# Performance work log

Measured on AMD Instinct MI355X. Metric: run time of the kernel, lower is better.

The kernel has to match this reference:

```python
import jax, jax.numpy as jnp
import numpy as np
import math

B, T, M, C, H = 2, 2048, 77, 512, 8
D = C // H  # head dim = 64


def setup_inputs() -> dict:
    key = jax.random.key(0)
    ks = jax.random.split(key, 20)
    s = 0.02
    inp = {
        "x": jax.random.normal(ks[0], (B, T, C), jnp.float32),
        "c": jax.random.normal(ks[1], (B, M, C), jnp.float32),
        # causal mask for self-attention (masked_fill where == 0)
        "attn_mask": jnp.tril(jnp.ones((T, T), jnp.int32))[None, None],
        "padding_mask": jnp.ones((B, M), jnp.int32),
    }
    names = ["Wq", "Wk", "Wv", "Wkc", "Wvc", "Wg1", "Wg2", "Wp"]
    for i, n in enumerate(names):
        inp[n] = jax.random.normal(ks[2 + i], (C, C), jnp.float32) * s
        inp["b" + n[1:]] = jnp.zeros((C,), jnp.float32)
    return inp


def _heads(t):
    # [B, S, C] -> [B, S, H, D]
    return t.reshape(t.shape[0], t.shape[1], H, D)


def reference(x, c, attn_mask, padding_mask,
              Wq, bq, Wk, bk, Wv, bv, Wkc, bkc, Wvc, bvc,
              Wg1, bg1, Wg2, bg2, Wp, bp):
    scale = 1.0 / math.sqrt(D)
    q = _heads(x @ Wq + bq)      # [B,T,H,D]
    k = _heads(x @ Wk + bk)      # [B,T,H,D]
    v = _heads(x @ Wv + bv)
    k_c = _heads(c @ Wkc + bkc)  # [B,M,H,D]
    v_c = _heads(c @ Wvc + bvc)

    # self-attention branch
    att = jnp.einsum("bthd,bshd->bhts", q, k) * scale   # [B,H,T,T]
    att = jnp.where(attn_mask == 0, -jnp.inf, att)
    att = jax.nn.softmax(att, axis=-1)
    y = jnp.einsum("bhts,bshd->bthd", att, v).reshape(B, T, C)

    # cross-attention branch to condition c
    att_c = jnp.einsum("bthd,bmhd->bhtm", q, k_c) * scale  # [B,H,T,M]
    att_c = jnp.where(padding_mask[:, None, None, :] == 0, -jnp.inf, att_c)
    att_c = jax.nn.softmax(att_c, axis=-1)
    y_c = jnp.einsum("bhtm,bmhd->bthd", att_c, v_c).reshape(B, T, C)

    # sigmoid gating fusion (note: gates cross-multiply branches, per source)
    gate_self = jax.nn.sigmoid(y @ Wg1 + bg1)
    gate_c = jax.nn.sigmoid(y_c @ Wg2 + bg2)
    y = gate_self * y_c + gate_c * y
    return y @ Wp + bp
```

## Files before the change

kernel.cpp:

```cpp
#include <hip/hip_runtime.h>
#include <hip/hip_bf16.h>
#include <math.h>

#define BB 2
#define TT 2048
#define MM 77
#define CC 512
#define HH 8
#define DD 64

typedef short bf16x8 __attribute__((ext_vector_type(8)));
typedef float f32x4  __attribute__((ext_vector_type(4)));

static __device__ __forceinline__ unsigned short f2bf(float x) {
    __hip_bfloat16 h = __float2bfloat16(x);
    return *reinterpret_cast<unsigned short*>(&h);
}
static __device__ __forceinline__ float bf2f(unsigned short u) {
    unsigned int v = ((unsigned int)u) << 16;
    return *reinterpret_cast<float*>(&v);
}

__global__ __launch_bounds__(256)
void wconv8(const float* __restrict__ w0, const float* __restrict__ w1,
            const float* __restrict__ w2, const float* __restrict__ w3,
            const float* __restrict__ w4, const float* __restrict__ w5,
            const float* __restrict__ w6, const float* __restrict__ w7,
            unsigned short* __restrict__ outbase)
{
    const float* W;
    switch (blockIdx.z) {
        case 0: W = w0; break; case 1: W = w1; break;
        case 2: W = w2; break; case 3: W = w3; break;
        case 4: W = w4; break; case 5: W = w5; break;
        case 6: W = w6; break; default: W = w7; break;
    }
    unsigned short* Wp = outbase + (size_t)blockIdx.z * 512 * 512;
    const int k0 = blockIdx.x * 64;
    const int n0 = blockIdx.y * 64;
    const int tid = threadIdx.x;
    __shared__ unsigned short t[64 * 72];

    #pragma unroll
    for (int it = 0; it < 4; ++it) {
        const int e = tid + 256 * it;
        const int r  = e >> 4;
        const int c4 = (e & 15) * 4;
        const float4 v = *(const float4*)(W + (size_t)(k0 + r) * 512 + n0 + c4);
        t[(c4 + 0) * 72 + r] = f2bf(v.x);
        t[(c4 + 1) * 72 + r] = f2bf(v.y);
        t[(c4 + 2) * 72 + r] = f2bf(v.z);
        t[(c4 + 3) * 72 + r] = f2bf(v.w);
    }
    __syncthreads();
    #pragma unroll
    for (int it = 0; it < 2; ++it) {
        const int e    = tid + 256 * it;
        const int gl   = e >> 7;
        const int ktl  = (e >> 6) & 1;
        const int lane = e & 63;
        const int l15  = lane & 15;
        const int q    = lane >> 4;
        const int4 v = *(const int4*)&t[(gl * 16 + l15) * 72 + ktl * 32 + q * 8];
        const int G  = (n0 >> 4) + gl;
        const int KT = (k0 >> 5) + ktl;
        *(int4*)(Wp + ((size_t)(G * 16 + KT) * 64 + lane) * 8) = v;
    }
}

__global__ __launch_bounds__(256)
void proj_all(const float* __restrict__ x, const float* __restrict__ cin,
              const unsigned short* __restrict__ Wt8,
              const float* __restrict__ bq, const float* __restrict__ bk,
              const float* __restrict__ bv, const float* __restrict__ bkc,
              const float* __restrict__ bvc,
              unsigned short* __restrict__ qb, unsigned short* __restrict__ kcb)
{
    __shared__ unsigned short As[2 * 16 * 64 * 8];

    const int tid = threadIdx.x;
    int b = blockIdx.x;
    const float* Ap; const unsigned short* Wtp;
    const float *bb0, *bb1, *bb2;
    unsigned short* outb;
    int row0, colb, N, S, whichStride;
    float oscale;
    if (b < 768) {
        row0 = (b & 127) * 32; colb = (b >> 7) * 256;
        Ap = x; Wtp = Wt8; N = BB * TT; S = TT;
        whichStride = 2097152; oscale = 0.125f;
        outb = qb; bb0 = bq; bb1 = bk; bb2 = bv;
    } else {
        b -= 768;
        row0 = (b % 5) * 32; colb = (b / 5) * 256;
        Ap = cin; Wtp = Wt8 + 3 * 262144; N = BB * MM; S = MM;
        whichStride = 131072; oscale = 1.0f;
        outb = kcb; bb0 = bkc; bb1 = bvc; bb2 = nullptr;
    }

    {
        const int r    = tid >> 3;
        const int rg   = r >> 4;
        const int l15r = r & 15;
        const int seg  = (tid & 7) * 64;
        const int gr   = row0 + r;
        unsigned short tmp[64];
        #pragma unroll
        for (int j = 0; j < 16; ++j) {
            float4 v = (gr < N) ? *(const float4*)(Ap + (size_t)gr * 512 + seg + j * 4)
                                : make_float4(0.f, 0.f, 0.f, 0.f);
            tmp[j*4+0] = f2bf(v.x); tmp[j*4+1] = f2bf(v.y);
            tmp[j*4+2] = f2bf(v.z); tmp[j*4+3] = f2bf(v.w);
        }
        #pragma unroll
        for (int jb = 0; jb < 8; ++jb) {
            const int k  = seg + jb * 8;
            const int kt = k >> 5;
            const int q  = (k >> 3) & 3;
            *(int4*)&As[((rg * 16 + kt) * 64 + q * 16 + l15r) * 8] = *(int4*)&tmp[jb*8];
        }
    }
    __syncthreads();

    const int wv   = tid >> 6;
    const int lane = tid & 63;
    const int l15  = lane & 15;
    const int quad = lane >> 4;
    const int wc   = colb + wv * 64;
    const int wcg  = wc >> 4;

    f32x4 acc[2][4];
    #pragma unroll
    for (int mi = 0; mi < 2; ++mi)
        #pragma unroll
        for (int ni = 0; ni < 4; ++ni) acc[mi][ni] = (f32x4){0.f, 0.f, 0.f, 0.f};

    bf16x8 b0v[4], b1v[4], b2v[4];
    #pragma unroll
    for (int ni = 0; ni < 4; ++ni) {
        b0v[ni] = *(const bf16x8*)(Wtp + (((size_t)(wcg + ni) * 16 + 0) << 9) + lane * 8);
        b1v[ni] = *(const bf16x8*)(Wtp + (((size_t)(wcg + ni) * 16 + 1) << 9) + lane * 8);
    }

    for (int kt = 0; kt < 16; ++kt) {
        if (kt + 2 < 16) {
            #pragma unroll
            for (int ni = 0; ni < 4; ++ni)
                b2v[ni] = *(const bf16x8*)(Wtp + (((size_t)(wcg + ni) * 16 + kt + 2) << 9) + lane * 8);
        }
        const bf16x8 a0 = *(const bf16x8*)&As[((0 * 16 + kt) * 64 + lane) * 8];
        const bf16x8 a1 = *(const bf16x8*)&As[((1 * 16 + kt) * 64 + lane) * 8];
        #pragma unroll
        for (int ni = 0; ni < 4; ++ni) {
            acc[0][ni] = __builtin_amdgcn_mfma_f32_16x16x32_bf16(a0, b0v[ni], acc[0][ni], 0, 0, 0);
            acc[1][ni] = __builtin_amdgcn_mfma_f32_16x16x32_bf16(a1, b0v[ni], acc[1][ni], 0, 0, 0);
        }
        #pragma unroll
        for (int ni = 0; ni < 4; ++ni) { b0v[ni] = b1v[ni]; b1v[ni] = b2v[ni]; }
    }

    const int which = wc >> 9;
    const float* bsel = (which == 0) ? bb0 : ((which == 1) ? bb1 : bb2);
    const float sc = (which == 0) ? oscale : 1.f;
    unsigned short* dst = outb + (size_t)which * whichStride;

    float bvv[4];
    #pragma unroll
    for (int ni = 0; ni < 4; ++ni)
        bvv[ni] = bsel[(wc + ni * 16 + l15) & 511];

    #pragma unroll
    for (int mi = 0; mi < 2; ++mi) {
        #pragma unroll
        for (int reg = 0; reg < 4; ++reg) {
            const int row = row0 + mi * 16 + quad * 4 + reg;
            if (row >= N) continue;
            const int b_ = row / S;
            const int s_ = row - b_ * S;
            #pragma unroll
            for (int ni = 0; ni < 4; ++ni) {
                const float v = (acc[mi][ni][reg] + bvv[ni]) * sc;
                const int cl = (wc + ni * 16 + l15) & 511;
                dst[((size_t)(b_ * HH + (cl >> 6)) * S + s_) * DD + (cl & 63)] = f2bf(v);
            }
        }
    }
}

template<int ACT, int OUT, int AMODE>
__global__ __launch_bounds__(256)
void gemm_rs(const void* __restrict__ A0, const void* __restrict__ A1,
             const void* __restrict__ A2, const void* __restrict__ A3,
             const unsigned short* __restrict__ Wt,
             const float* __restrict__ b0, const float* __restrict__ b1,
             void* __restrict__ out0, void* __restrict__ out1,
             int N, int NC)
{
    __shared__ unsigned short As[2 * 16 * 64 * 8];

    const int tid  = threadIdx.x;
    const int z    = blockIdx.z;
    const int row0 = blockIdx.x * 32;
    const int colb = blockIdx.y * 256;
    const void* Ap = z ? A1 : A0;

    {
        const int r    = tid >> 3;
        const int rg   = r >> 4;
        const int l15r = r & 15;
        const int seg  = (tid & 7) * 64;
        const int gr   = row0 + r;
        unsigned short tmp[64];
        if (AMODE == 2) {
            #pragma unroll
            for (int jb = 0; jb < 8; ++jb) {
                unsigned short a[8], bq_[8], c[8], d[8];
                if (gr < N) {
                    const size_t off = (size_t)gr * 512 + seg + jb * 8;
                    *(int4*)a   = *(const int4*)((const unsigned short*)A0 + off);
                    *(int4*)bq_ = *(const int4*)((const unsigned short*)A1 + off);
                    *(int4*)c   = *(const int4*)((const unsigned short*)A2 + off);
                    *(int4*)d   = *(const int4*)((const unsigned short*)A3 + off);
                    #pragma unroll
                    for (int k = 0; k < 8; ++k)
                        tmp[jb*8+k] = f2bf(bf2f(a[k]) * bf2f(bq_[k]) + bf2f(c[k]) * bf2f(d[k]));
                } else {
                    #pragma unroll
                    for (int k = 0; k < 8; ++k) tmp[jb*8+k] = 0;
                }
            }
        } else {
            const unsigned short* Ab = (const unsigned short*)Ap;
            #pragma unroll
            for (int jb = 0; jb < 8; ++jb) {
                int4 v = (gr < N) ? *(const int4*)(Ab + (size_t)gr * 512 + seg + jb * 8)
                                  : make_int4(0, 0, 0, 0);
                *(int4*)&tmp[jb*8] = v;
            }
        }
        #pragma unroll
        for (int jb = 0; jb < 8; ++jb) {
            const int k  = seg + jb * 8;
            const int kt = k >> 5;
            const int q  = (k >> 3) & 3;
            *(int4*)&As[((rg * 16 + kt) * 64 + q * 16 + l15r) * 8] = *(int4*)&tmp[jb*8];
        }
    }
    __syncthreads();

    const int wv   = tid >> 6;
    const int lane = tid & 63;
    const int l15  = lane & 15;
    const int quad = lane >> 4;
    const int wc   = colb + wv * 64;
    const int wcg  = wc >> 4;

    f32x4 acc[2][4];
    #pragma unroll
    for (int mi = 0; mi < 2; ++mi)
        #pragma unroll
        for (int ni = 0; ni < 4; ++ni) acc[mi][ni] = (f32x4){0.f, 0.f, 0.f, 0.f};

    const unsigned short* Wz = Wt + (size_t)z * NC;

    bf16x8 b0v[4], b1v[4], b2v[4];
    #pragma unroll
    for (int ni = 0; ni < 4; ++ni) {
        b0v[ni] = *(const bf16x8*)(Wz + (((size_t)(wcg + ni) * 16 + 0) << 9) + lane * 8);
        b1v[ni] = *(const bf16x8*)(Wz + (((size_t)(wcg + ni) * 16 + 1) << 9) + lane * 8);
    }

    for (int kt = 0; kt < 16; ++kt) {
        if (kt + 2 < 16) {
            #pragma unroll
            for (int ni = 0; ni < 4; ++ni)
                b2v[ni] = *(const bf16x8*)(Wz + (((size_t)(wcg + ni) * 16 + kt + 2) << 9) + lane * 8);
        }
        const bf16x8 a0 = *(const bf16x8*)&As[((0 * 16 + kt) * 64 + lane) * 8];
        const bf16x8 a1 = *(const bf16x8*)&As[((1 * 16 + kt) * 64 + lane) * 8];
        #pragma unroll
        for (int ni = 0; ni < 4; ++ni) {
            acc[0][ni] = __builtin_amdgcn_mfma_f32_16x16x32_bf16(a0, b0v[ni], acc[0][ni], 0, 0, 0);
            acc[1][ni] = __builtin_amdgcn_mfma_f32_16x16x32_bf16(a1, b0v[ni], acc[1][ni], 0, 0, 0);
        }
        #pragma unroll
        for (int ni = 0; ni < 4; ++ni) { b0v[ni] = b1v[ni]; b1v[ni] = b2v[ni]; }
    }

    const float* bsel = ((OUT == 1) && z) ? b1 : b0;
    float bvv[4];
    #pragma unroll
    for (int ni = 0; ni < 4; ++ni)
        bvv[ni] = bsel[(wc + ni * 16 + l15) & 511];

    #pragma unroll
    for (int mi = 0; mi < 2; ++mi) {
        #pragma unroll
        for (int reg = 0; reg < 4; ++reg) {
            const int row = row0 + mi * 16 + quad * 4 + reg;
            if (row >= N) continue;
            #pragma unroll
            for (int ni = 0; ni < 4; ++ni) {
                float v = acc[mi][ni][reg] + bvv[ni];
                if (ACT == 1) v = 1.f / (1.f + __expf(-v));
                const int col = wc + ni * 16 + l15;
                if (OUT == 0) {
                    ((float*)out0)[(size_t)row * 512 + col] = v;
                } else {
                    unsigned short* dst = (unsigned short*)(z ? out1 : out0);
                    dst[(size_t)row * 512 + col] = f2bf(v);
                }
            }
        }
    }
}

__global__ __launch_bounds__(256)
void transpose_all(const unsigned short* __restrict__ vin, unsigned short* __restrict__ vout,
                   const unsigned short* __restrict__ cin_, unsigned short* __restrict__ cout_)
{
    const int bx = blockIdx.x;
    const int bh = blockIdx.y;
    const unsigned short* in; unsigned short* outp;
    int S, W, s0;
    if (bx < 32) { in = vin;  outp = vout;  S = TT; W = TT;  s0 = bx * 64; }
    else         { in = cin_; outp = cout_; S = MM; W = 128; s0 = (bx - 32) * 64; }

    const int tid = threadIdx.x;
    __shared__ unsigned short t[64 * 80];

    #pragma unroll
    for (int it = 0; it < 2; ++it) {
        const int e = tid + 256 * it;
        const int row = e >> 3;
        const int blk = e & 7;
        int4 v = make_int4(0, 0, 0, 0);
        const int s = s0 + row;
        if (s < S) v = *(const int4*)(in + ((size_t)bh * S + s) * 64 + blk * 8);
        *(int4*)&t[row * 80 + ((blk ^ (row & 7)) * 8)] = v;
    }
    __syncthreads();
    #pragma unroll
    for (int it = 0; it < 2; ++it) {
        const int e = tid + 256 * it;
        const int d  = e >> 3;
        const int kb = e & 7;
        const int key0 = s0 + kb * 8;
        if (key0 < W) {
            unsigned short tmp[8];
            #pragma unroll
            for (int j = 0; j < 8; ++j) {
                const int kl = kb * 8 + j;
                tmp[j] = t[kl * 80 + (((d >> 3) ^ (kl & 7)) * 8) + (d & 7)];
            }
            *(int4*)(outp + ((size_t)bh * 64 + d) * W + key0) = *(int4*)tmp;
        }
    }
}

__global__ __launch_bounds__(256)
void attn_all(const unsigned short* __restrict__ Qh,
              const unsigned short* __restrict__ Kh,
              const unsigned short* __restrict__ Vth,
              unsigned short* __restrict__ yout,
              const unsigned short* __restrict__ Kch,
              const unsigned short* __restrict__ Vtch,
              unsigned short* __restrict__ ycout)
{
    int lin = blockIdx.x;
    int causal, S_kv, W, bh, qt;
    const unsigned short *Kb, *Vb;
    unsigned short* outp;
    if (lin < 512) {
        causal = 1; S_kv = TT; W = TT;
        bh = (lin & 7) | (((lin >> 3) & 1) << 3);
        const int qtr = lin >> 4;
        qt = (qtr < 16) ? (31 - qtr) : (qtr - 16);
        Kb = Kh + (size_t)bh * S_kv * 64;
        Vb = Vth + (size_t)bh * 64 * W;
        outp = yout;
    } else {
        lin -= 512;
        causal = 0; S_kv = MM; W = 128;
        bh = (lin & 7) | (((lin >> 3) & 1) << 3);
        qt = lin >> 4;
        Kb = Kch + (size_t)bh * S_kv * 64;
        Vb = Vtch + (size_t)bh * 64 * W;
        outp = ycout;
    }
    const int n_kt = causal ? (qt + 1) : 2;

    const int tid  = threadIdx.x;
    const int wv   = tid >> 6;
    const int lane = tid & 63;
    const int l15  = lane & 15;
    const int quad = lane >> 4;

    __shared__ unsigned short Ks[2][64 * 80];
    __shared__ unsigned short Vs[2][64 * 80];
    __shared__ unsigned short PT[4 * 16 * 72];

    const int t0 = qt * 64 + wv * 16;
    const unsigned short* qptr = Qh + ((size_t)bh * TT + t0 + l15) * 64 + quad * 8;
    const bf16x8 qb0 = *(const bf16x8*)(qptr);
    const bf16x8 qb1 = *(const bf16x8*)(qptr + 32);

    f32x4 Oacc[4];
    #pragma unroll
    for (int dt = 0; dt < 4; ++dt) Oacc[dt] = (f32x4){0.f, 0.f, 0.f, 0.f};
    float l = 0.f;

    int4 kR[2], vR[2];
    {
        #pragma unroll
        for (int it = 0; it < 2; ++it) {
            const int e = tid + 256 * it;
            const int row = e >> 3, blk = e & 7;
            kR[it] = (row < S_kv)
                ? *(const int4*)(Kb + (size_t)row * 64 + blk * 8) : make_int4(0,0,0,0);
            vR[it] = (blk * 8 < W)
                ? *(const int4*)(Vb + (size_t)row * W + blk * 8) : make_int4(0,0,0,0);
        }
        #pragma unroll
        for (int it = 0; it < 2; ++it) {
            const int e = tid + 256 * it;
            const int row = e >> 3, blk = e & 7;
            *(int4*)&Ks[0][row * 80 + ((blk ^ (row & 7)) * 8)] = kR[it];
            *(int4*)&Vs[0][row * 80 + ((blk ^ (row & 7)) * 8)] = vR[it];
        }
    }
    __syncthreads();

    for (int kt = 0; kt < n_kt; ++kt) {
        const int buf = kt & 1;
        const int s0 = kt * 64;

        if (kt + 1 < n_kt) {
            const int s1 = (kt + 1) * 64;
            #pragma unroll
            for (int it = 0; it < 2; ++it) {
                const int e = tid + 256 * it;
                const int row = e >> 3, blk = e & 7;
                const int s = s1 + row;
                kR[it] = (s < S_kv)
                    ? *(const int4*)(Kb + (size_t)s * 64 + blk * 8) : make_int4(0,0,0,0);
                vR[it] = (s1 + blk * 8 < W)
                    ? *(const int4*)(Vb + (size_t)row * W + s1 + blk * 8) : make_int4(0,0,0,0);
            }
        }

        f32x4 sacc[4];
        #pragma unroll
        for (int mt = 0; mt < 4; ++mt) {
            const int krow = 16 * mt + l15;
            const bf16x8 ka0 = *(const bf16x8*)&Ks[buf][krow * 80 + (((quad    ) ^ (krow & 7)) * 8)];
            const bf16x8 ka1 = *(const bf16x8*)&Ks[buf][krow * 80 + (((quad + 4) ^ (krow & 7)) * 8)];
            sacc[mt] = (f32x4){0.f, 0.f, 0.f, 0.f};
            sacc[mt] = __builtin_amdgcn_mfma_f32_16x16x32_bf16(ka0, qb0, sacc[mt], 0, 0, 0);
            sacc[mt] = __builtin_amdgcn_mfma_f32_16x16x32_bf16(ka1, qb1, sacc[mt], 0, 0, 0);
        }

        float sv[16];
        #pragma unroll
        for (int mt = 0; mt < 4; ++mt)
            #pragma unroll
            for (int reg = 0; reg < 4; ++reg)
                sv[mt * 4 + reg] = sacc[mt][reg];

        const bool cmask = (causal && kt == qt);
        if (cmask || (s0 + 64 > S_kv)) {
            const int lim = cmask ? (t0 + l15) : 0x7fffffff;
            #pragma unroll
            for (int mt = 0; mt < 4; ++mt)
                #pragma unroll
                for (int reg = 0; reg < 4; ++reg) {
                    const int kg = s0 + 16 * mt + quad * 4 + reg;
                    if (kg > lim || kg >= S_kv) sv[mt * 4 + reg] = -INFINITY;
                }
        }

        float p[16], psum = 0.f;
        #pragma unroll
        for (int i = 0; i < 16; ++i) { p[i] = __expf(sv[i]); psum += p[i]; }
        psum += __shfl_xor(psum, 16);
        psum += __shfl_xor(psum, 32);
        l += psum;

        unsigned short* ptw = &PT[wv * 16 * 72 + l15 * 72];
        #pragma unroll
        for (int mt = 0; mt < 4; ++mt) {
            ushort4 u;
            u.x = f2bf(p[mt * 4 + 0]); u.y = f2bf(p[mt * 4 + 1]);
            u.z = f2bf(p[mt * 4 + 2]); u.w = f2bf(p[mt * 4 + 3]);
            *(ushort4*)(ptw + 16 * mt + quad * 4) = u;
        }
        const bf16x8 pb0 = *(const bf16x8*)(ptw + quad * 8);
        const bf16x8 pb1 = *(const bf16x8*)(ptw + quad * 8 + 32);

        #pragma unroll
        for (int dt = 0; dt < 4; ++dt) {
            const int vrow = 16 * dt + l15;
            const bf16x8 va0 = *(const bf16x8*)&Vs[buf][vrow * 80 + (((quad    ) ^ (vrow & 7)) * 8)];
            const bf16x8 va1 = *(const bf16x8*)&Vs[buf][vrow * 80 + (((quad + 4) ^ (vrow & 7)) * 8)];
            Oacc[dt] = __builtin_amdgcn_mfma_f32_16x16x32_bf16(va0, pb0, Oacc[dt], 0, 0, 0);
            Oacc[dt] = __builtin_amdgcn_mfma_f32_16x16x32_bf16(va1, pb1, Oacc[dt], 0, 0, 0);
        }

        if (kt + 1 < n_kt) {
            const int nbuf = buf ^ 1;
            #pragma unroll
            for (int it = 0; it < 2; ++it) {
                const int e = tid + 256 * it;
                const int row = e >> 3, blk = e & 7;
                *(int4*)&Ks[nbuf][row * 80 + ((blk ^ (row & 7)) * 8)] = kR[it];
                *(int4*)&Vs[nbuf][row * 80 + ((blk ^ (row & 7)) * 8)] = vR[it];
            }
        }
        __syncthreads();
    }

    const int b = bh >> 3, h = bh & 7;
    const float inv_l = 1.f / l;
    const int t = t0 + l15;
    unsigned short* ob = outp + ((size_t)b * TT + t) * CC + h * DD + quad * 4;
    #pragma unroll
    for (int dt = 0; dt < 4; ++dt) {
        ushort4 u;
        u.x = f2bf(Oacc[dt][0] * inv_l);
        u.y = f2bf(Oacc[dt][1] * inv_l);
        u.z = f2bf(Oacc[dt][2] * inv_l);
        u.w = f2bf(Oacc[dt][3] * inv_l);
        *(ushort4*)(ob + 16 * dt) = u;
    }
}

extern "C" void kernel_launch(void* const* d_in, const int* in_sizes, int n_in,
                              void* d_out, int out_size, void* d_ws, size_t ws_size,
                              hipStream_t stream)
{
    const float* x   = (const float*)d_in[0];
    const float* cin = (const float*)d_in[1];
    const float* Wq  = (const float*)d_in[4];   const float* bq  = (const float*)d_in[5];
    const float* Wk  = (const float*)d_in[6];   const float* bk  = (const float*)d_in[7];
    const float* Wv  = (const float*)d_in[8];   const float* bv  = (const float*)d_in[9];
    const float* Wkc = (const float*)d_in[10];  const float* bkc = (const float*)d_in[11];
    const float* Wvc = (const float*)d_in[12];  const float* bvc = (const float*)d_in[13];
    const float* Wg1 = (const float*)d_in[14];  const float* bg1 = (const float*)d_in[15];
    const float* Wg2 = (const float*)d_in[16];  const float* bg2 = (const float*)d_in[17];
    const float* Wp  = (const float*)d_in[18];  const float* bp  = (const float*)d_in[19];

    float* out = (float*)d_out;
    char*  w   = (char*)d_ws;
    const size_t MB = 1024 * 1024;

    unsigned short* Wt8  = (unsigned short*)(w);
    unsigned short* qb   = (unsigned short*)(w + 4  * MB);
    unsigned short* kb   = (unsigned short*)(w + 8  * MB);
    unsigned short* vb   = (unsigned short*)(w + 12 * MB);
    unsigned short* vtb  = (unsigned short*)(w + 16 * MB);
    unsigned short* yb   = (unsigned short*)(w + 20 * MB);
    unsigned short* ycb  = (unsigned short*)(w + 24 * MB);
    unsigned short* g1b  = (unsigned short*)(w + 28 * MB);
    unsigned short* g2b  = (unsigned short*)(w + 32 * MB);
    unsigned short* kcb  = (unsigned short*)(w + 40 * MB);
    unsigned short* vcb  = (unsigned short*)(w + 40 * MB + 256 * 1024);
    unsigned short* vtcb = (unsigned short*)(w + 40 * MB + 512 * 1024);

    const dim3 blk(256);

    wconv8<<<dim3(8, 8, 8), blk, 0, stream>>>(Wq, Wk, Wv, Wkc, Wvc, Wg1, Wg2, Wp, Wt8);

    proj_all<<<dim3(788), blk, 0, stream>>>(
        x, cin, Wt8, bq, bk, bv, bkc, bvc, qb, kcb);

    transpose_all<<<dim3(34, BB * HH), blk, 0, stream>>>(vb, vtb, vcb, vtcb);

    attn_all<<<dim3(1024), blk, 0, stream>>>(qb, kb, vtb, yb, kcb, vtcb, ycb);

    gemm_rs<1, 1, 0><<<dim3(128, 2, 2), blk, 0, stream>>>(
        yb, ycb, nullptr, nullptr, Wt8 + 5 * 262144, bg1, bg2, g1b, g2b,
        BB * TT, 262144);

    gemm_rs<0, 0, 2><<<dim3(128, 2), blk, 0, stream>>>(
        g1b, ycb, g2b, yb, Wt8 + 7 * 262144, bp, nullptr, out, nullptr,
        BB * TT, 0);
}
```

Measured before the change: 203.9 us.

## Fuse V transpose into projection epilogue and enlarge GEMM row tiles

```diff
diff --git a/kernel.cpp b/kernel.cpp
--- a/kernel.cpp
+++ b/kernel.cpp
@@ -74,32 +74,33 @@
               const float* __restrict__ bq, const float* __restrict__ bk,
               const float* __restrict__ bv, const float* __restrict__ bkc,
               const float* __restrict__ bvc,
-              unsigned short* __restrict__ qb, unsigned short* __restrict__ kcb)
+              unsigned short* __restrict__ qb,
+              unsigned short* __restrict__ vtb,
+              unsigned short* __restrict__ kcb,
+              unsigned short* __restrict__ vtcb)
 {
-    __shared__ unsigned short As[2 * 16 * 64 * 8];
+    __shared__ unsigned short As[4 * 16 * 64 * 8];
 
     const int tid = threadIdx.x;
     int b = blockIdx.x;
     const float* Ap; const unsigned short* Wtp;
     const float *bb0, *bb1, *bb2;
-    unsigned short* outb;
-    int row0, colb, N, S, whichStride;
-    float oscale;
-    if (b < 768) {
-        row0 = (b & 127) * 32; colb = (b >> 7) * 256;
-        Ap = x; Wtp = Wt8; N = BB * TT; S = TT;
-        whichStride = 2097152; oscale = 0.125f;
-        outb = qb; bb0 = bq; bb1 = bk; bb2 = bv;
+    int row0, colb, N, isSelf;
+    if (b < 384) {
+        isSelf = 1;
+        row0 = (b & 63) * 64; colb = (b >> 6) * 256;
+        Ap = x; Wtp = Wt8; N = BB * TT;
+        bb0 = bq; bb1 = bk; bb2 = bv;
     } else {
-        b -= 768;
-        row0 = (b % 5) * 32; colb = (b / 5) * 256;
-        Ap = cin; Wtp = Wt8 + 3 * 262144; N = BB * MM; S = MM;
-        whichStride = 131072; oscale = 1.0f;
-        outb = kcb; bb0 = bkc; bb1 = bvc; bb2 = nullptr;
-    }
-
-    {
-        const int r    = tid >> 3;
+        b -= 384; isSelf = 0;
+        row0 = (b % 3) * 64; colb = (b / 3) * 256;
+        Ap = cin; Wtp = Wt8 + 3 * 262144; N = BB * MM;
+        bb0 = bkc; bb1 = bvc; bb2 = nullptr;
+    }
+
+    #pragma unroll
+    for (int half = 0; half < 2; ++half) {
+        const int r    = half * 32 + (tid >> 3);
         const int rg   = r >> 4;
         const int l15r = r & 15;
         const int seg  = (tid & 7) * 64;
@@ -129,9 +130,9 @@
     const int wc   = colb + wv * 64;
     const int wcg  = wc >> 4;
 
-    f32x4 acc[2][4];
-    #pragma unroll
-    for (int mi = 0; mi < 2; ++mi)
+    f32x4 acc[4][4];
+    #pragma unroll
+    for (int mi = 0; mi < 4; ++mi)
         #pragma unroll
         for (int ni = 0; ni < 4; ++ni) acc[mi][ni] = (f32x4){0.f, 0.f, 0.f, 0.f};
 
@@ -148,46 +149,98 @@
             for (int ni = 0; ni < 4; ++ni)
                 b2v[ni] = *(const bf16x8*)(Wtp + (((size_t)(wcg + ni) * 16 + kt + 2) << 9) + lane * 8);
         }
-        const bf16x8 a0 = *(const bf16x8*)&As[((0 * 16 + kt) * 64 + lane) * 8];
-        const bf16x8 a1 = *(const bf16x8*)&As[((1 * 16 + kt) * 64 + lane) * 8];
-        #pragma unroll
-        for (int ni = 0; ni < 4; ++ni) {
-            acc[0][ni] = __builtin_amdgcn_mfma_f32_16x16x32_bf16(a0, b0v[ni], acc[0][ni], 0, 0, 0);
-            acc[1][ni] = __builtin_amdgcn_mfma_f32_16x16x32_bf16(a1, b0v[ni], acc[1][ni], 0, 0, 0);
-        }
+        bf16x8 a[4];
+        #pragma unroll
+        for (int mi = 0; mi < 4; ++mi)
+            a[mi] = *(const bf16x8*)&As[((mi * 16 + kt) * 64 + lane) * 8];
+        #pragma unroll
+        for (int ni = 0; ni < 4; ++ni)
+            #pragma unroll
+            for (int mi = 0; mi < 4; ++mi)
+                acc[mi][ni] = __builtin_amdgcn_mfma_f32_16x16x32_bf16(a[mi], b0v[ni], acc[mi][ni], 0, 0, 0);
         #pragma unroll
         for (int ni = 0; ni < 4; ++ni) { b0v[ni] = b1v[ni]; b1v[ni] = b2v[ni]; }
     }
 
     const int which = wc >> 9;
     const float* bsel = (which == 0) ? bb0 : ((which == 1) ? bb1 : bb2);
-    const float sc = (which == 0) ? oscale : 1.f;
-    unsigned short* dst = outb + (size_t)which * whichStride;
+    const float sc = (isSelf && which == 0) ? 0.125f : 1.f;
 
     float bvv[4];
     #pragma unroll
     for (int ni = 0; ni < 4; ++ni)
         bvv[ni] = bsel[(wc + ni * 16 + l15) & 511];
 
-    #pragma unroll
-    for (int mi = 0; mi < 2; ++mi) {
-        #pragma unroll
-        for (int reg = 0; reg < 4; ++reg) {
-            const int row = row0 + mi * 16 + quad * 4 + reg;
-            if (row >= N) continue;
-            const int b_ = row / S;
-            const int s_ = row - b_ * S;
-            #pragma unroll
-            for (int ni = 0; ni < 4; ++ni) {
-                const float v = (acc[mi][ni][reg] + bvv[ni]) * sc;
-                const int cl = (wc + ni * 16 + l15) & 511;
-                dst[((size_t)(b_ * HH + (cl >> 6)) * S + s_) * DD + (cl & 63)] = f2bf(v);
-            }
-        }
+    if (isSelf) {
+        const int b_ = row0 >> 11;
+        const int t0 = row0 & 2047;
+        const int h  = (wc & 511) >> 6;
+        __syncthreads();
+        unsigned short* TL = (unsigned short*)As + wv * (64 * 72);
+        if (which < 2) {
+            #pragma unroll
+            for (int mi = 0; mi < 4; ++mi)
+                #pragma unroll
+                for (int ni = 0; ni < 4; ++ni)
+                    #pragma unroll
+                    for (int reg = 0; reg < 4; ++reg) {
+                        const int t = mi * 16 + quad * 4 + reg;
+                        const int d = ni * 16 + l15;
+                        TL[t * 72 + d] = f2bf((acc[mi][ni][reg] + bvv[ni]) * sc);
+                    }
+            unsigned short* dst = qb + (size_t)which * 2097152
+                                + (((size_t)b_ * 8 + h) * 2048 + t0) * 64;
+            #pragma unroll
+            for (int it = 0; it < 8; ++it) {
+                const int t = it * 8 + (lane >> 3);
+                *(int4*)(dst + (size_t)t * 64 + (lane & 7) * 8)
+                    = *(const int4*)&TL[t * 72 + (lane & 7) * 8];
+            }
+        } else {
+            #pragma unroll
+            for (int mi = 0; mi < 4; ++mi)
+                #pragma unroll
+                for (int ni = 0; ni < 4; ++ni) {
+                    ushort4 u;
+                    u.x = f2bf(acc[mi][ni][0] + bvv[ni]);
+                    u.y = f2bf(acc[mi][ni][1] + bvv[ni]);
+                    u.z = f2bf(acc[mi][ni][2] + bvv[ni]);
+                    u.w = f2bf(acc[mi][ni][3] + bvv[ni]);
+                    const int d = ni * 16 + l15;
+                    *(ushort4*)&TL[d * 72 + mi * 16 + quad * 4] = u;
+                }
+            unsigned short* dst = vtb + (((size_t)b_ * 8 + h) * 64) * 2048 + t0;
+            #pragma unroll
+            for (int it = 0; it < 8; ++it) {
+                const int d = it * 8 + (lane >> 3);
+                *(int4*)(dst + (size_t)d * 2048 + (lane & 7) * 8)
+                    = *(const int4*)&TL[d * 72 + (lane & 7) * 8];
+            }
+        }
+    } else {
+        #pragma unroll
+        for (int mi = 0; mi < 4; ++mi)
+            #pragma unroll
+            for (int reg = 0; reg < 4; ++reg) {
+                const int row = row0 + mi * 16 + quad * 4 + reg;
+                if (row >= N) continue;
+                const int b_ = (row >= MM) ? 1 : 0;
+                const int m_ = row - b_ * MM;
+                #pragma unroll
+                for (int ni = 0; ni < 4; ++ni) {
+                    const float v = acc[mi][ni][reg] + bvv[ni];
+                    const int cl = (wc + ni * 16 + l15) & 511;
+                    const int h = cl >> 6, d = cl & 63;
+                    if (which == 0)
+                        kcb[(((size_t)b_ * 8 + h) * 77 + m_) * 64 + d] = f2bf(v);
+                    else
+                        vtcb[(((size_t)b_ * 8 + h) * 64 + d) * 128 + m_] = f2bf(v);
+                }
+            }
     }
 }
 
-template<int ACT, int OUT, int AMODE>
+template<int ACT, int OUT, int AMODE, int MI>
 __global__ __launch_bounds__(256)
 void gemm_rs(const void* __restrict__ A0, const void* __restrict__ A1,
              const void* __restrict__ A2, const void* __restrict__ A3,
@@ -196,16 +249,17 @@
              void* __restrict__ out0, void* __restrict__ out1,
              int N, int NC)
 {
-    __shared__ unsigned short As[2 * 16 * 64 * 8];
+    __shared__ unsigned short As[MI * 16 * 64 * 8];
 
     const int tid  = threadIdx.x;
     const int z    = blockIdx.z;
-    const int row0 = blockIdx.x * 32;
+    const int row0 = blockIdx.x * (MI * 16);
     const int colb = blockIdx.y * 256;
     const void* Ap = z ? A1 : A0;
 
-    {
-        const int r    = tid >> 3;
+    #pragma unroll
+    for (int half = 0; half < MI / 2; ++half) {
+        const int r    = half * 32 + (tid >> 3);
         const int rg   = r >> 4;
         const int l15r = r & 15;
         const int seg  = (tid & 7) * 64;
@@ -255,9 +309,9 @@
     const int wc   = colb + wv * 64;
     const int wcg  = wc >> 4;
 
-    f32x4 acc[2][4];
-    #pragma unroll
-    for (int mi = 0; mi < 2; ++mi)
+    f32x4 acc[MI][4];
+    #pragma unroll
+    for (int mi = 0; mi < MI; ++mi)
         #pragma unroll
         for (int ni = 0; ni < 4; ++ni) acc[mi][ni] = (f32x4){0.f, 0.f, 0.f, 0.f};
 
@@ -276,13 +330,15 @@
             for (int ni = 0; ni < 4; ++ni)
                 b2v[ni] = *(const bf16x8*)(Wz + (((size_t)(wcg + ni) * 16 + kt + 2) << 9) + lane * 8);
         }
-        const bf16x8 a0 = *(const bf16x8*)&As[((0 * 16 + kt) * 64 + lane) * 8];
-        const bf16x8 a1 = *(const bf16x8*)&As[((1 * 16 + kt) * 64 + lane) * 8];
-        #pragma unroll
-        for (int ni = 0; ni < 4; ++ni) {
-            acc[0][ni] = __builtin_amdgcn_mfma_f32_16x16x32_bf16(a0, b0v[ni], acc[0][ni], 0, 0, 0);
-            acc[1][ni] = __builtin_amdgcn_mfma_f32_16x16x32_bf16(a1, b0v[ni], acc[1][ni], 0, 0, 0);
-        }
+        bf16x8 a[MI];
+        #pragma unroll
+        for (int mi = 0; mi < MI; ++mi)
+            a[mi] = *(const bf16x8*)&As[((mi * 16 + kt) * 64 + lane) * 8];
+        #pragma unroll
+        for (int ni = 0; ni < 4; ++ni)
+            #pragma unroll
+            for (int mi = 0; mi < MI; ++mi)
+                acc[mi][ni] = __builtin_amdgcn_mfma_f32_16x16x32_bf16(a[mi], b0v[ni], acc[mi][ni], 0, 0, 0);
         #pragma unroll
         for (int ni = 0; ni < 4; ++ni) { b0v[ni] = b1v[ni]; b1v[ni] = b2v[ni]; }
     }
@@ -294,7 +350,7 @@
         bvv[ni] = bsel[(wc + ni * 16 + l15) & 511];
 
     #pragma unroll
-    for (int mi = 0; mi < 2; ++mi) {
+    for (int mi = 0; mi < MI; ++mi) {
         #pragma unroll
         for (int reg = 0; reg < 4; ++reg) {
             const int row = row0 + mi * 16 + quad * 4 + reg;
@@ -311,49 +367,6 @@
                     dst[(size_t)row * 512 + col] = f2bf(v);
                 }
             }
-        }
-    }
-}
-
-__global__ __launch_bounds__(256)
-void transpose_all(const unsigned short* __restrict__ vin, unsigned short* __restrict__ vout,
-                   const unsigned short* __restrict__ cin_, unsigned short* __restrict__ cout_)
-{
-    const int bx = blockIdx.x;
-    const int bh = blockIdx.y;
-    const unsigned short* in; unsigned short* outp;
-    int S, W, s0;
-    if (bx < 32) { in = vin;  outp = vout;  S = TT; W = TT;  s0 = bx * 64; }
-    else         { in = cin_; outp = cout_; S = MM; W = 128; s0 = (bx - 32) * 64; }
-
-    const int tid = threadIdx.x;
-    __shared__ unsigned short t[64 * 80];
-
-    #pragma unroll
-    for (int it = 0; it < 2; ++it) {
-        const int e = tid + 256 * it;
-        const int row = e >> 3;
-        const int blk = e & 7;
-        int4 v = make_int4(0, 0, 0, 0);
-        const int s = s0 + row;
-        if (s < S) v = *(const int4*)(in + ((size_t)bh * S + s) * 64 + blk * 8);
-        *(int4*)&t[row * 80 + ((blk ^ (row & 7)) * 8)] = v;
-    }
-    __syncthreads();
-    #pragma unroll
-    for (int it = 0; it < 2; ++it) {
-        const int e = tid + 256 * it;
-        const int d  = e >> 3;
-        const int kb = e & 7;
-        const int key0 = s0 + kb * 8;
-        if (key0 < W) {
-            unsigned short tmp[8];
-            #pragma unroll
-            for (int j = 0; j < 8; ++j) {
-                const int kl = kb * 8 + j;
-                tmp[j] = t[kl * 80 + (((d >> 3) ^ (kl & 7)) * 8) + (d & 7)];
-            }
-            *(int4*)(outp + ((size_t)bh * 64 + d) * W + key0) = *(int4*)tmp;
         }
     }
 }
@@ -389,6 +402,7 @@
         outp = ycout;
     }
     const int n_kt = causal ? (qt + 1) : 2;
+    const int vlim = causal ? TT : MM;
 
     const int tid  = threadIdx.x;
     const int wv   = tid >> 6;
@@ -444,8 +458,18 @@
                 const int s = s1 + row;
                 kR[it] = (s < S_kv)
                     ? *(const int4*)(Kb + (size_t)s * 64 + blk * 8) : make_int4(0,0,0,0);
-                vR[it] = (s1 + blk * 8 < W)
-                    ? *(const int4*)(Vb + (size_t)row * W + s1 + blk * 8) : make_int4(0,0,0,0);
+                const int c0 = s1 + blk * 8;
+                int4 vv = make_int4(0, 0, 0, 0);
+                if (c0 < vlim) {
+                    vv = *(const int4*)(Vb + (size_t)row * W + c0);
+                    if (c0 + 8 > vlim) {
+                        unsigned short* sp = (unsigned short*)&vv;
+                        #pragma unroll
+                        for (int j = 0; j < 8; ++j)
+                            if (c0 + j >= vlim) sp[j] = 0;
+                    }
+                }
+                vR[it] = vv;
             }
         }
 
@@ -555,33 +579,29 @@
 
     unsigned short* Wt8  = (unsigned short*)(w);
     unsigned short* qb   = (unsigned short*)(w + 4  * MB);
-    unsigned short* kb   = (unsigned short*)(w + 8  * MB);
-    unsigned short* vb   = (unsigned short*)(w + 12 * MB);
-    unsigned short* vtb  = (unsigned short*)(w + 16 * MB);
+    unsigned short* vtb  = (unsigned short*)(w + 12 * MB);
     unsigned short* yb   = (unsigned short*)(w + 20 * MB);
     unsigned short* ycb  = (unsigned short*)(w + 24 * MB);
     unsigned short* g1b  = (unsigned short*)(w + 28 * MB);
     unsigned short* g2b  = (unsigned short*)(w + 32 * MB);
     unsigned short* kcb  = (unsigned short*)(w + 40 * MB);
-    unsigned short* vcb  = (unsigned short*)(w + 40 * MB + 256 * 1024);
-    unsigned short* vtcb = (unsigned short*)(w + 40 * MB + 512 * 1024);
+    unsigned short* vtcb = (unsigned short*)(w + 40 * MB + 256 * 1024);
 
     const dim3 blk(256);
 
     wconv8<<<dim3(8, 8, 8), blk, 0, stream>>>(Wq, Wk, Wv, Wkc, Wvc, Wg1, Wg2, Wp, Wt8);
 
-    proj_all<<<dim3(788), blk, 0, stream>>>(
-        x, cin, Wt8, bq, bk, bv, bkc, bvc, qb, kcb);
-
-    transpose_all<<<dim3(34, BB * HH), blk, 0, stream>>>(vb, vtb, vcb, vtcb);
-
-    attn_all<<<dim3(1024), blk, 0, stream>>>(qb, kb, vtb, yb, kcb, vtcb, ycb);
-
-    gemm_rs<1, 1, 0><<<dim3(128, 2, 2), blk, 0, stream>>>(
+    proj_all<<<dim3(396), blk, 0, stream>>>(
+        x, cin, Wt8, bq, bk, bv, bkc, bvc, qb, vtb, kcb, vtcb);
+
+    attn_all<<<dim3(1024), blk, 0, stream>>>(
+        qb, qb + 2097152, vtb, yb, kcb, vtcb, ycb);
+
+    gemm_rs<1, 1, 0, 4><<<dim3(64, 2, 2), blk, 0, stream>>>(
         yb, ycb, nullptr, nullptr, Wt8 + 5 * 262144, bg1, bg2, g1b, g2b,
         BB * TT, 262144);
 
-    gemm_rs<0, 0, 2><<<dim3(128, 2), blk, 0, stream>>>(
+    gemm_rs<0, 0, 2, 2><<<dim3(128, 2), blk, 0, stream>>>(
         g1b, ycb, g2b, yb, Wt8 + 7 * 262144, bp, nullptr, out, nullptr,
         BB * TT, 0);
 }
```

Result: slower. 224.5 us (+10.1%).
